# Kernel tuning notes

Hardware: AMD Instinct MI355X
Metric: run time of the kernel (lower is better)

Reference implementation:

```python
import jax, jax.numpy as jnp
import numpy as np

B, INPUT_DIM, D_MODEL, NHEAD = 1024, 1024, 1024, 16
D_HEAD = D_MODEL // NHEAD


def unitnorm(v, eps=1e-12):
    # torch F.normalize(dim=-1): v / max(||v||_2, eps)
    n = jnp.sqrt(jnp.sum(v * v, axis=-1, keepdims=True))
    return v / jnp.maximum(n, eps)


def setup_inputs() -> dict:
    key = jax.random.key(0)
    ks = jax.random.split(key, 8)
    d_in = D_MODEL + INPUT_DIM
    s = 1.0 / np.sqrt(d_in)  # torch Linear default init scale
    return {
        "x": jax.random.normal(ks[0], (B, INPUT_DIM), jnp.float32),
        "h": jax.random.normal(ks[1], (B, D_MODEL), jnp.float32),
        "AM": jax.random.normal(ks[2], (B, NHEAD, D_HEAD, D_HEAD), jnp.float32) * 0.1,
        "Wqkv_w": jax.random.normal(ks[3], (d_in, 3 * D_MODEL), jnp.float32) * s,
        "Wqkv_b": jnp.zeros((3 * D_MODEL,), jnp.float32),
        "Ww_w": jax.random.normal(ks[4], (d_in, NHEAD), jnp.float32) * s,
        "Ww_b": jnp.zeros((NHEAD,), jnp.float32),
        "Wr_w": jax.random.normal(ks[5], (d_in, NHEAD), jnp.float32) * s,
        "Wr_b": jnp.zeros((NHEAD,), jnp.float32),
    }


def reference(x, h, AM, Wqkv_w, Wqkv_b, Ww_w, Ww_b, Wr_w, Wr_b):
    b = x.shape[0]
    nhead = Ww_w.shape[1]
    d_head = Wqkv_w.shape[1] // (3 * nhead)
    xh = jnp.concatenate([x, h], axis=-1)                 # [B, d_model+input_dim]
    qkv = (xh @ Wqkv_w + Wqkv_b).reshape(b, 3, nhead, d_head)
    q = unitnorm(qkv[:, 0])                                # [B, n, d]
    k = unitnorm(qkv[:, 1])
    v = qkv[:, 2]
    w = jax.nn.sigmoid(xh @ Ww_w + Ww_b)                   # [B, n]
    v_r = jnp.einsum('bnvq,bnq->bnv', AM, k)               # read: AM @ k
    vp = w[:, :, None] * (v - v_r)                         # gated delta
    AM_new = AM + jnp.einsum('bnq,bnv->bnvq', k, vp)       # outer-product write
    r = jax.nn.sigmoid(xh @ Wr_w + Wr_b)                   # [B, n]
    h_new = jnp.einsum('bnvq,bnq->bnv', AM_new, q) * r[:, :, None]
    return h_new.reshape(b, -1), AM_new
```

## Files before the change

### kernel.cpp

```cpp
#include <hip/hip_runtime.h>
#include <math.h>

#define B_SZ      1024
#define INPUT_DIM 1024
#define D_MODEL   1024
#define NHEAD     16
#define D_HEAD    64
#define D_IN      2048
#define N_QKV     3072

__global__ __launch_bounds__(256) void gemm_qkv_kernel(
    const float* __restrict__ x, const float* __restrict__ h,
    const float* __restrict__ W, const float* __restrict__ bias,
    float* __restrict__ out)
{
    __shared__ float As[16][68];
    __shared__ float Bs[16][132];

    const int tid = threadIdx.x;
    const int ty  = tid >> 4;
    const int tx  = tid & 15;
    const int m0  = blockIdx.y * 64;
    const int n0  = blockIdx.x * 128;

    const int arow = tid >> 2;
    const int acol = (tid & 3) * 4;
    const int brow = tid >> 5;
    const int bcol = (tid & 31) * 4;

    float c[4][8];
#pragma unroll
    for (int i = 0; i < 4; ++i)
#pragma unroll
        for (int j = 0; j < 8; ++j) c[i][j] = 0.f;

    for (int kt = 0; kt < D_IN; kt += 16) {
        const int colA = kt + acol;
        const float* asrc = (colA < INPUT_DIM)
            ? (x + (size_t)(m0 + arow) * INPUT_DIM + colA)
            : (h + (size_t)(m0 + arow) * D_MODEL  + (colA - INPUT_DIM));
        float4 av  = *reinterpret_cast<const float4*>(asrc);
        float4 bv0 = *reinterpret_cast<const float4*>(W + (size_t)(kt + brow    ) * N_QKV + n0 + bcol);
        float4 bv1 = *reinterpret_cast<const float4*>(W + (size_t)(kt + brow + 8) * N_QKV + n0 + bcol);

        __syncthreads();
        As[acol + 0][arow] = av.x;
        As[acol + 1][arow] = av.y;
        As[acol + 2][arow] = av.z;
        As[acol + 3][arow] = av.w;
        *reinterpret_cast<float4*>(&Bs[brow    ][bcol]) = bv0;
        *reinterpret_cast<float4*>(&Bs[brow + 8][bcol]) = bv1;
        __syncthreads();

#pragma unroll
        for (int k = 0; k < 16; ++k) {
            float4 a  = *reinterpret_cast<const float4*>(&As[k][ty * 4]);
            float4 b0 = *reinterpret_cast<const float4*>(&Bs[k][tx * 8]);
            float4 b1 = *reinterpret_cast<const float4*>(&Bs[k][tx * 8 + 4]);
            float avv[4] = {a.x, a.y, a.z, a.w};
            float bvv[8] = {b0.x, b0.y, b0.z, b0.w, b1.x, b1.y, b1.z, b1.w};
#pragma unroll
            for (int i = 0; i < 4; ++i)
#pragma unroll
                for (int j = 0; j < 8; ++j)
                    c[i][j] = fmaf(avv[i], bvv[j], c[i][j]);
        }
    }

    float bvals[8];
#pragma unroll
    for (int j = 0; j < 8; ++j) bvals[j] = bias[n0 + tx * 8 + j];
#pragma unroll
    for (int i = 0; i < 4; ++i) {
        const int row = m0 + ty * 4 + i;
        float* dst = out + (size_t)row * N_QKV + n0 + tx * 8;
        float4 o0, o1;
        o0.x = c[i][0] + bvals[0]; o0.y = c[i][1] + bvals[1];
        o0.z = c[i][2] + bvals[2]; o0.w = c[i][3] + bvals[3];
        o1.x = c[i][4] + bvals[4]; o1.y = c[i][5] + bvals[5];
        o1.z = c[i][6] + bvals[6]; o1.w = c[i][7] + bvals[7];
        *reinterpret_cast<float4*>(dst)     = o0;
        *reinterpret_cast<float4*>(dst + 4) = o1;
    }
}

__global__ __launch_bounds__(256) void gemm_wr_kernel(
    const float* __restrict__ x, const float* __restrict__ h,
    const float* __restrict__ Ww, const float* __restrict__ Wwb,
    const float* __restrict__ Wr, const float* __restrict__ Wrb,
    float* __restrict__ w_out, float* __restrict__ r_out)
{
    const int b     = blockIdx.x;
    const int tid   = threadIdx.x;
    const int j     = tid & 31;
    const int slice = tid >> 5;
    const int col   = j & 15;
    const float* Wm = (j < 16) ? Ww : Wr;

    const int k0 = slice * 256;
    const float* src = (k0 < INPUT_DIM) ? (x + (size_t)b * INPUT_DIM + k0)
                                        : (h + (size_t)b * D_MODEL + (k0 - INPUT_DIM));
    float acc = 0.f;
#pragma unroll 8
    for (int i = 0; i < 256; ++i)
        acc = fmaf(src[i], Wm[(size_t)(k0 + i) * NHEAD + col], acc);

    __shared__ float red[8][32];
    red[slice][j] = acc;
    __syncthreads();
    if (tid < 32) {
        float s = 0.f;
#pragma unroll
        for (int i = 0; i < 8; ++i) s += red[i][tid];
        const int cc = tid & 15;
        if (tid < 16) {
            s += Wwb[cc];
            w_out[(size_t)b * NHEAD + cc] = 1.f / (1.f + expf(-s));
        } else {
            s += Wrb[cc];
            r_out[(size_t)b * NHEAD + cc] = 1.f / (1.f + expf(-s));
        }
    }
}

__global__ __launch_bounds__(64) void am_update_kernel(
    const float* __restrict__ qkv, const float* __restrict__ AM,
    const float* __restrict__ w_arr, const float* __restrict__ r_arr,
    float* __restrict__ h_out, float* __restrict__ am_out)
{
    const int bn   = blockIdx.x;
    const int b    = bn >> 4;
    const int n    = bn & 15;
    const int lane = threadIdx.x;

    const float* row = qkv + (size_t)b * N_QKV;
    float qv = row[             n * 64 + lane];
    float kv = row[D_MODEL    + n * 64 + lane];
    float vv = row[2 * D_MODEL + n * 64 + lane];

    float qs = qv * qv, ks = kv * kv;
#pragma unroll
    for (int off = 32; off > 0; off >>= 1) {
        qs += __shfl_xor(qs, off);
        ks += __shfl_xor(ks, off);
    }
    const float qn = qv / fmaxf(sqrtf(qs), 1e-12f);
    const float kn = kv / fmaxf(sqrtf(ks), 1e-12f);

    __shared__ float qL[64], kL[64];
    qL[lane] = qn;
    kL[lane] = kn;
    __syncthreads();

    const float4* amr = reinterpret_cast<const float4*>(AM + (size_t)bn * 4096 + lane * 64);
    float4 am[16];
#pragma unroll
    for (int i = 0; i < 16; ++i) am[i] = amr[i];

    float vr = 0.f;
#pragma unroll
    for (int i = 0; i < 16; ++i) {
        float4 kk = *reinterpret_cast<const float4*>(&kL[i * 4]);
        vr = fmaf(am[i].x, kk.x, vr);
        vr = fmaf(am[i].y, kk.y, vr);
        vr = fmaf(am[i].z, kk.z, vr);
        vr = fmaf(am[i].w, kk.w, vr);
    }

    const float wv = w_arr[bn];
    const float rv = r_arr[bn];
    const float vp = wv * (vv - vr);

    float hv = 0.f;
    float4* amo = reinterpret_cast<float4*>(am_out + (size_t)bn * 4096 + lane * 64);
#pragma unroll
    for (int i = 0; i < 16; ++i) {
        float4 kk = *reinterpret_cast<const float4*>(&kL[i * 4]);
        float4 qq = *reinterpret_cast<const float4*>(&qL[i * 4]);
        float4 a  = am[i];
        a.x = fmaf(vp, kk.x, a.x);
        a.y = fmaf(vp, kk.y, a.y);
        a.z = fmaf(vp, kk.z, a.z);
        a.w = fmaf(vp, kk.w, a.w);
        hv = fmaf(a.x, qq.x, hv);
        hv = fmaf(a.y, qq.y, hv);
        hv = fmaf(a.z, qq.z, hv);
        hv = fmaf(a.w, qq.w, hv);
        amo[i] = a;
    }
    h_out[(size_t)b * D_MODEL + n * 64 + lane] = hv * rv;
}

extern "C" void kernel_launch(void* const* d_in, const int* in_sizes, int n_in,
                              void* d_out, int out_size, void* d_ws, size_t ws_size,
                              hipStream_t stream)
{
    const float* x      = (const float*)d_in[0];
    const float* h      = (const float*)d_in[1];
    const float* AM     = (const float*)d_in[2];
    const float* Wqkv_w = (const float*)d_in[3];
    const float* Wqkv_b = (const float*)d_in[4];
    const float* Ww_w   = (const float*)d_in[5];
    const float* Ww_b   = (const float*)d_in[6];
    const float* Wr_w   = (const float*)d_in[7];
    const float* Wr_b   = (const float*)d_in[8];

    float* out    = (float*)d_out;
    float* h_out  = out;
    float* am_out = out + (size_t)B_SZ * D_MODEL;

    float* ws    = (float*)d_ws;
    float* qkv   = ws;
    float* w_arr = ws + (size_t)B_SZ * N_QKV;
    float* r_arr = w_arr + (size_t)B_SZ * NHEAD;

    dim3 g1(N_QKV / 128, B_SZ / 64);
    gemm_qkv_kernel<<<g1, dim3(256), 0, stream>>>(x, h, Wqkv_w, Wqkv_b, qkv);
    gemm_wr_kernel<<<dim3(B_SZ), dim3(256), 0, stream>>>(x, h, Ww_w, Ww_b, Wr_w, Wr_b, w_arr, r_arr);
    am_update_kernel<<<dim3(B_SZ * NHEAD), dim3(64), 0, stream>>>(qkv, AM, w_arr, r_arr, h_out, am_out);
}
```

Baseline: 741.6 us.

## Use split-bf16 MFMA for QKV GEMM and coalesce AM update loads

Replaces the FP32 SIMT QKV GEMM with a bf16 MFMA GEMM. The fp32 accuracy is approximated by splitting each operand into hi and lo bf16 parts and issuing three MFMAs per tile. Pre-pass kernels convert and transpose the activations and weights into workspace every call, which adds memory traffic. The AM update kernel is restructured so each wave reads AM with coalesced float4 accesses and uses shuffle reductions instead of per-lane row reads, with four heads per block.

```diff
diff --git a/kernel.cpp b/kernel.cpp
--- a/kernel.cpp
+++ b/kernel.cpp
@@ -6,82 +6,177 @@
 #define D_MODEL   1024
 #define NHEAD     16
 #define D_HEAD    64
-#define D_IN      2048
+#define K_DIM     2048
 #define N_QKV     3072
 
-__global__ __launch_bounds__(256) void gemm_qkv_kernel(
+typedef __bf16 bf16x8 __attribute__((ext_vector_type(8)));
+typedef float  f32x4  __attribute__((ext_vector_type(4)));
+
+__device__ __forceinline__ unsigned short f2bf(float f) {
+    unsigned u = __builtin_bit_cast(unsigned, f);
+    u += 0x7fffu + ((u >> 16) & 1u);
+    return (unsigned short)(u >> 16);
+}
+__device__ __forceinline__ float bf2f(unsigned short s) {
+    unsigned u = ((unsigned)s) << 16;
+    return __builtin_bit_cast(float, u);
+}
+__device__ __forceinline__ uint4 pack8(const unsigned short* s) {
+    uint4 r;
+    r.x = s[0] | ((unsigned)s[1] << 16);
+    r.y = s[2] | ((unsigned)s[3] << 16);
+    r.z = s[4] | ((unsigned)s[5] << 16);
+    r.w = s[6] | ((unsigned)s[7] << 16);
+    return r;
+}
+
+__global__ __launch_bounds__(256) void conv_a_kernel(
     const float* __restrict__ x, const float* __restrict__ h,
-    const float* __restrict__ W, const float* __restrict__ bias,
-    float* __restrict__ out)
-{
-    __shared__ float As[16][68];
-    __shared__ float Bs[16][132];
-
-    const int tid = threadIdx.x;
-    const int ty  = tid >> 4;
-    const int tx  = tid & 15;
-    const int m0  = blockIdx.y * 64;
-    const int n0  = blockIdx.x * 128;
-
-    const int arow = tid >> 2;
-    const int acol = (tid & 3) * 4;
-    const int brow = tid >> 5;
-    const int bcol = (tid & 31) * 4;
-
-    float c[4][8];
+    unsigned short* __restrict__ Ahi, unsigned short* __restrict__ Alo)
+{
+    const int m = blockIdx.x;
+    const int t = threadIdx.x;
+    const float* src = (t < 128) ? (x + (size_t)m * INPUT_DIM + t * 8)
+                                 : (h + (size_t)m * D_MODEL + t * 8 - INPUT_DIM);
+    float4 v0 = ((const float4*)src)[0];
+    float4 v1 = ((const float4*)src)[1];
+    float f[8] = {v0.x, v0.y, v0.z, v0.w, v1.x, v1.y, v1.z, v1.w};
+    unsigned short hi[8], lo[8];
+#pragma unroll
+    for (int j = 0; j < 8; ++j) {
+        hi[j] = f2bf(f[j]);
+        lo[j] = f2bf(f[j] - bf2f(hi[j]));
+    }
+    const size_t off = (size_t)m * K_DIM + t * 8;
+    *reinterpret_cast<uint4*>(Ahi + off) = pack8(hi);
+    *reinterpret_cast<uint4*>(Alo + off) = pack8(lo);
+}
+
+__global__ __launch_bounds__(256) void conv_b_kernel(
+    const float* __restrict__ W,
+    unsigned short* __restrict__ Bthi, unsigned short* __restrict__ Btlo)
+{
+    __shared__ float tile[64][65];
+    const int n0 = blockIdx.x * 64;
+    const int k0 = blockIdx.y * 64;
+    const int t  = threadIdx.x;
+
+    const int lrow = t >> 4;
+    const int lcol = (t & 15) * 4;
+#pragma unroll
+    for (int p = 0; p < 4; ++p) {
+        const int r = p * 16 + lrow;
+        float4 v = *reinterpret_cast<const float4*>(W + (size_t)(k0 + r) * N_QKV + n0 + lcol);
+        tile[r][lcol + 0] = v.x;
+        tile[r][lcol + 1] = v.y;
+        tile[r][lcol + 2] = v.z;
+        tile[r][lcol + 3] = v.w;
+    }
+    __syncthreads();
+
+    const int nl = t >> 2;
+    const int kc = (t & 3) * 16;
+    unsigned short hi[16], lo[16];
+#pragma unroll
+    for (int i = 0; i < 16; ++i) {
+        float f = tile[kc + i][nl];
+        hi[i] = f2bf(f);
+        lo[i] = f2bf(f - bf2f(hi[i]));
+    }
+    const size_t off = (size_t)(n0 + nl) * K_DIM + k0 + kc;
+    *reinterpret_cast<uint4*>(Bthi + off)     = pack8(hi);
+    *reinterpret_cast<uint4*>(Bthi + off + 8) = pack8(hi + 8);
+    *reinterpret_cast<uint4*>(Btlo + off)     = pack8(lo);
+    *reinterpret_cast<uint4*>(Btlo + off + 8) = pack8(lo + 8);
+}
+
+__global__ __launch_bounds__(256) void gemm_qkv_mfma(
+    const unsigned short* __restrict__ Ahi, const unsigned short* __restrict__ Alo,
+    const unsigned short* __restrict__ Bthi, const unsigned short* __restrict__ Btlo,
+    const float* __restrict__ bias, float* __restrict__ out)
+{
+    __shared__ unsigned short sAh[128 * 64];
+    __shared__ unsigned short sAl[128 * 64];
+    __shared__ unsigned short sBh[128 * 64];
+    __shared__ unsigned short sBl[128 * 64];
+
+    const int t    = threadIdx.x;
+    const int lane = t & 63;
+    const int wid  = t >> 6;
+    const int wm   = wid >> 1;
+    const int wn   = wid & 1;
+    const int m0   = blockIdx.y * 128;
+    const int n0   = blockIdx.x * 128;
+
+    f32x4 acc[4][4];
 #pragma unroll
     for (int i = 0; i < 4; ++i)
 #pragma unroll
-        for (int j = 0; j < 8; ++j) c[i][j] = 0.f;
-
-    for (int kt = 0; kt < D_IN; kt += 16) {
-        const int colA = kt + acol;
-        const float* asrc = (colA < INPUT_DIM)
-            ? (x + (size_t)(m0 + arow) * INPUT_DIM + colA)
-            : (h + (size_t)(m0 + arow) * D_MODEL  + (colA - INPUT_DIM));
-        float4 av  = *reinterpret_cast<const float4*>(asrc);
-        float4 bv0 = *reinterpret_cast<const float4*>(W + (size_t)(kt + brow    ) * N_QKV + n0 + bcol);
-        float4 bv1 = *reinterpret_cast<const float4*>(W + (size_t)(kt + brow + 8) * N_QKV + n0 + bcol);
-
+        for (int j = 0; j < 4; ++j) acc[i][j] = (f32x4){0.f, 0.f, 0.f, 0.f};
+
+    for (int kt = 0; kt < K_DIM; kt += 64) {
+        uint4 ra[4], rb[4], rc[4], rd[4];
+#pragma unroll
+        for (int p = 0; p < 4; ++p) {
+            const int pi = p * 256 + t;
+            const int R  = pi >> 3;
+            const int cs = pi & 7;
+            const int cl = cs ^ (R & 7);
+            const size_t ga = (size_t)(m0 + R) * K_DIM + kt + cl * 8;
+            const size_t gb = (size_t)(n0 + R) * K_DIM + kt + cl * 8;
+            ra[p] = *reinterpret_cast<const uint4*>(Ahi  + ga);
+            rb[p] = *reinterpret_cast<const uint4*>(Alo  + ga);
+            rc[p] = *reinterpret_cast<const uint4*>(Bthi + gb);
+            rd[p] = *reinterpret_cast<const uint4*>(Btlo + gb);
+        }
         __syncthreads();
-        As[acol + 0][arow] = av.x;
-        As[acol + 1][arow] = av.y;
-        As[acol + 2][arow] = av.z;
-        As[acol + 3][arow] = av.w;
-        *reinterpret_cast<float4*>(&Bs[brow    ][bcol]) = bv0;
-        *reinterpret_cast<float4*>(&Bs[brow + 8][bcol]) = bv1;
+#pragma unroll
+        for (int p = 0; p < 4; ++p) {
+            const int pi = p * 256 + t;
+            *reinterpret_cast<uint4*>(&sAh[pi * 8]) = ra[p];
+            *reinterpret_cast<uint4*>(&sAl[pi * 8]) = rb[p];
+            *reinterpret_cast<uint4*>(&sBh[pi * 8]) = rc[p];
+            *reinterpret_cast<uint4*>(&sBl[pi * 8]) = rd[p];
+        }
         __syncthreads();
 
 #pragma unroll
-        for (int k = 0; k < 16; ++k) {
-            float4 a  = *reinterpret_cast<const float4*>(&As[k][ty * 4]);
-            float4 b0 = *reinterpret_cast<const float4*>(&Bs[k][tx * 8]);
-            float4 b1 = *reinterpret_cast<const float4*>(&Bs[k][tx * 8 + 4]);
-            float avv[4] = {a.x, a.y, a.z, a.w};
-            float bvv[8] = {b0.x, b0.y, b0.z, b0.w, b1.x, b1.y, b1.z, b1.w};
-#pragma unroll
-            for (int i = 0; i < 4; ++i)
-#pragma unroll
-                for (int j = 0; j < 8; ++j)
-                    c[i][j] = fmaf(avv[i], bvv[j], c[i][j]);
-        }
-    }
-
-    float bvals[8];
-#pragma unroll
-    for (int j = 0; j < 8; ++j) bvals[j] = bias[n0 + tx * 8 + j];
-#pragma unroll
-    for (int i = 0; i < 4; ++i) {
-        const int row = m0 + ty * 4 + i;
-        float* dst = out + (size_t)row * N_QKV + n0 + tx * 8;
-        float4 o0, o1;
-        o0.x = c[i][0] + bvals[0]; o0.y = c[i][1] + bvals[1];
-        o0.z = c[i][2] + bvals[2]; o0.w = c[i][3] + bvals[3];
-        o1.x = c[i][4] + bvals[4]; o1.y = c[i][5] + bvals[5];
-        o1.z = c[i][6] + bvals[6]; o1.w = c[i][7] + bvals[7];
-        *reinterpret_cast<float4*>(dst)     = o0;
-        *reinterpret_cast<float4*>(dst + 4) = o1;
-    }
+        for (int kk = 0; kk < 2; ++kk) {
+            bf16x8 ah[4], al[4], bh[4], bl[4];
+#pragma unroll
+            for (int i = 0; i < 4; ++i) {
+                const int RA = wm * 64 + i * 16 + (lane & 15);
+                const int ca = (kk * 4 + (lane >> 4)) ^ (RA & 7);
+                ah[i] = *reinterpret_cast<const bf16x8*>(&sAh[RA * 64 + ca * 8]);
+                al[i] = *reinterpret_cast<const bf16x8*>(&sAl[RA * 64 + ca * 8]);
+                const int RB = wn * 64 + i * 16 + (lane & 15);
+                const int cb = (kk * 4 + (lane >> 4)) ^ (RB & 7);
+                bh[i] = *reinterpret_cast<const bf16x8*>(&sBh[RB * 64 + cb * 8]);
+                bl[i] = *reinterpret_cast<const bf16x8*>(&sBl[RB * 64 + cb * 8]);
+            }
+#pragma unroll
+            for (int mi = 0; mi < 4; ++mi)
+#pragma unroll
+                for (int ni = 0; ni < 4; ++ni) {
+                    acc[mi][ni] = __builtin_amdgcn_mfma_f32_16x16x32_bf16(ah[mi], bh[ni], acc[mi][ni], 0, 0, 0);
+                    acc[mi][ni] = __builtin_amdgcn_mfma_f32_16x16x32_bf16(ah[mi], bl[ni], acc[mi][ni], 0, 0, 0);
+                    acc[mi][ni] = __builtin_amdgcn_mfma_f32_16x16x32_bf16(al[mi], bh[ni], acc[mi][ni], 0, 0, 0);
+                }
+        }
+    }
+
+#pragma unroll
+    for (int mi = 0; mi < 4; ++mi)
+#pragma unroll
+        for (int ni = 0; ni < 4; ++ni) {
+            const int col = n0 + wn * 64 + ni * 16 + (lane & 15);
+            const float bv = bias[col];
+#pragma unroll
+            for (int r = 0; r < 4; ++r) {
+                const int row = m0 + wm * 64 + mi * 16 + (lane >> 4) * 4 + r;
+                out[(size_t)row * N_QKV + col] = acc[mi][ni][r] + bv;
+            }
+        }
 }
 
 __global__ __launch_bounds__(256) void gemm_wr_kernel(
@@ -123,15 +218,16 @@
     }
 }
 
-__global__ __launch_bounds__(64) void am_update_kernel(
+__global__ __launch_bounds__(256) void am_update_kernel(
     const float* __restrict__ qkv, const float* __restrict__ AM,
     const float* __restrict__ w_arr, const float* __restrict__ r_arr,
     float* __restrict__ h_out, float* __restrict__ am_out)
 {
-    const int bn   = blockIdx.x;
+    const int wid  = threadIdx.x >> 6;
+    const int lane = threadIdx.x & 63;
+    const int bn   = blockIdx.x * 4 + wid;
     const int b    = bn >> 4;
     const int n    = bn & 15;
-    const int lane = threadIdx.x;
 
     const float* row = qkv + (size_t)b * N_QKV;
     float qv = row[             n * 64 + lane];
@@ -147,48 +243,58 @@
     const float qn = qv / fmaxf(sqrtf(qs), 1e-12f);
     const float kn = kv / fmaxf(sqrtf(ks), 1e-12f);
 
-    __shared__ float qL[64], kL[64];
-    qL[lane] = qn;
-    kL[lane] = kn;
-    __syncthreads();
-
-    const float4* amr = reinterpret_cast<const float4*>(AM + (size_t)bn * 4096 + lane * 64);
+    const int c = lane & 15;
+    const int g = lane >> 4;
+    float kk[4], qq[4];
+#pragma unroll
+    for (int j = 0; j < 4; ++j) {
+        kk[j] = __shfl(kn, 4 * c + j);
+        qq[j] = __shfl(qn, 4 * c + j);
+    }
+
+    const float4* amp = reinterpret_cast<const float4*>(AM + (size_t)bn * 4096);
     float4 am[16];
 #pragma unroll
-    for (int i = 0; i < 16; ++i) am[i] = amr[i];
-
-    float vr = 0.f;
-#pragma unroll
-    for (int i = 0; i < 16; ++i) {
-        float4 kk = *reinterpret_cast<const float4*>(&kL[i * 4]);
-        vr = fmaf(am[i].x, kk.x, vr);
-        vr = fmaf(am[i].y, kk.y, vr);
-        vr = fmaf(am[i].z, kk.z, vr);
-        vr = fmaf(am[i].w, kk.w, vr);
-    }
+    for (int i = 0; i < 16; ++i) am[i] = amp[i * 64 + lane];
+
+    float vr[16];
+#pragma unroll
+    for (int i = 0; i < 16; ++i)
+        vr[i] = am[i].x * kk[0] + am[i].y * kk[1] + am[i].z * kk[2] + am[i].w * kk[3];
+#pragma unroll
+    for (int off = 1; off < 16; off <<= 1)
+#pragma unroll
+        for (int i = 0; i < 16; ++i) vr[i] += __shfl_xor(vr[i], off);
 
     const float wv = w_arr[bn];
     const float rv = r_arr[bn];
-    const float vp = wv * (vv - vr);
-
-    float hv = 0.f;
-    float4* amo = reinterpret_cast<float4*>(am_out + (size_t)bn * 4096 + lane * 64);
+
+    float vel[16];
+#pragma unroll
+    for (int i = 0; i < 16; ++i) vel[i] = __shfl(vv, 4 * i + g);
+
+    float4* amo = reinterpret_cast<float4*>(am_out + (size_t)bn * 4096);
+    float hp[16];
 #pragma unroll
     for (int i = 0; i < 16; ++i) {
-        float4 kk = *reinterpret_cast<const float4*>(&kL[i * 4]);
-        float4 qq = *reinterpret_cast<const float4*>(&qL[i * 4]);
-        float4 a  = am[i];
-        a.x = fmaf(vp, kk.x, a.x);
-        a.y = fmaf(vp, kk.y, a.y);
-        a.z = fmaf(vp, kk.z, a.z);
-        a.w = fmaf(vp, kk.w, a.w);
-        hv = fmaf(a.x, qq.x, hv);
-        hv = fmaf(a.y, qq.y, hv);
-        hv = fmaf(a.z, qq.z, hv);
-        hv = fmaf(a.w, qq.w, hv);
-        amo[i] = a;
-    }
-    h_out[(size_t)b * D_MODEL + n * 64 + lane] = hv * rv;
+        const float vp = wv * (vel[i] - vr[i]);
+        float4 a = am[i];
+        a.x = fmaf(vp, kk[0], a.x);
+        a.y = fmaf(vp, kk[1], a.y);
+        a.z = fmaf(vp, kk[2], a.z);
+        a.w = fmaf(vp, kk[3], a.w);
+        hp[i] = a.x * qq[0] + a.y * qq[1] + a.z * qq[2] + a.w * qq[3];
+        amo[i * 64 + lane] = a;
+    }
+#pragma unroll
+    for (int off = 1; off < 16; off <<= 1)
+#pragma unroll
+        for (int i = 0; i < 16; ++i) hp[i] += __shfl_xor(hp[i], off);
+
+    float hsel = 0.f;
+#pragma unroll
+    for (int i = 0; i < 16; ++i) if (c == i) hsel = hp[i];
+    h_out[(size_t)b * D_MODEL + n * 64 + 4 * c + g] = hsel * rv;
 }
 
 extern "C" void kernel_launch(void* const* d_in, const int* in_sizes, int n_in,
@@ -211,11 +317,16 @@
 
     float* ws    = (float*)d_ws;
     float* qkv   = ws;
-    float* w_arr = ws + (size_t)B_SZ * N_QKV;
-    float* r_arr = w_arr + (size_t)B_SZ * NHEAD;
-
-    dim3 g1(N_QKV / 128, B_SZ / 64);
-    gemm_qkv_kernel<<<g1, dim3(256), 0, stream>>>(x, h, Wqkv_w, Wqkv_b, qkv);
+    float* w_arr = qkv + (size_t)B_SZ * N_QKV;
+    float* r_arr = w_arr + B_SZ * NHEAD;
+    unsigned short* Ahi  = (unsigned short*)(r_arr + B_SZ * NHEAD);
+    unsigned short* Alo  = Ahi + (size_t)B_SZ * K_DIM;
+    unsigned short* Bthi = Alo + (size_t)B_SZ * K_DIM;
+    unsigned short* Btlo = Bthi + (size_t)N_QKV * K_DIM;
+
+    conv_a_kernel<<<dim3(B_SZ), dim3(256), 0, stream>>>(x, h, Ahi, Alo);
+    conv_b_kernel<<<dim3(N_QKV / 64, K_DIM / 64), dim3(256), 0, stream>>>(Wqkv_w, Bthi, Btlo);
     gemm_wr_kernel<<<dim3(B_SZ), dim3(256), 0, stream>>>(x, h, Ww_w, Ww_b, Wr_w, Wr_b, w_arr, r_arr);
-    am_update_kernel<<<dim3(B_SZ * NHEAD), dim3(64), 0, stream>>>(qkv, AM, w_arr, r_arr, h_out, am_out);
-}
+    gemm_qkv_mfma<<<dim3(N_QKV / 128, B_SZ / 128), dim3(256), 0, stream>>>(Ahi, Alo, Bthi, Btlo, Wqkv_b, qkv);
+    am_update_kernel<<<dim3(B_SZ * NHEAD / 4), dim3(256), 0, stream>>>(qkv, AM, w_arr, r_arr, h_out, am_out);
+}
```

Result: faster. 661.0 us (-10.9%).
